# Kernel tuning notes

Hardware: AMD Instinct MI355X
Metric: run time of the kernel (lower is better)

Reference implementation:

```python
import jax, jax.numpy as jnp
import numpy as np

N_NODES = 50000
N_EDGES = 600000
D_IN = 128
D_HID = 128
D_OUT = 47
BN_EPS = 1e-5


def setup_inputs() -> dict:
    key = jax.random.key(0)
    ks = jax.random.split(key, 16)
    x = jax.random.normal(ks[0], (N_NODES, D_IN), dtype=jnp.float32)
    edge_index = jax.random.randint(ks[1], (2, N_EDGES), 0, N_NODES, dtype=jnp.int64)
    s = 0.05
    return {
        'x': x,
        'edge_index': edge_index,
        # SAGEConv layer 1: lin_l (neighbor agg, with bias), lin_r (root, no bias)
        'W1l': jax.random.normal(ks[2], (D_IN, D_HID), jnp.float32) * s,
        'b1': jnp.zeros((D_HID,), jnp.float32),
        'W1r': jax.random.normal(ks[3], (D_IN, D_HID), jnp.float32) * s,
        # layer 2
        'W2l': jax.random.normal(ks[4], (D_HID, D_HID), jnp.float32) * s,
        'b2': jnp.zeros((D_HID,), jnp.float32),
        'W2r': jax.random.normal(ks[5], (D_HID, D_HID), jnp.float32) * s,
        # layer 3
        'W3l': jax.random.normal(ks[6], (D_HID, D_OUT), jnp.float32) * s,
        'b3': jnp.zeros((D_OUT,), jnp.float32),
        'W3r': jax.random.normal(ks[7], (D_HID, D_OUT), jnp.float32) * s,
        # BatchNorm params (eval mode: running stats)
        'g1': jnp.ones((D_HID,), jnp.float32),
        'be1': jnp.zeros((D_HID,), jnp.float32),
        'm1': jax.random.normal(ks[8], (D_HID,), jnp.float32) * 0.1,
        'v1': jnp.ones((D_HID,), jnp.float32) + jax.random.uniform(ks[9], (D_HID,)) * 0.1,
        'g2': jnp.ones((D_HID,), jnp.float32),
        'be2': jnp.zeros((D_HID,), jnp.float32),
        'm2': jax.random.normal(ks[10], (D_HID,), jnp.float32) * 0.1,
        'v2': jnp.ones((D_HID,), jnp.float32) + jax.random.uniform(ks[11], (D_HID,)) * 0.1,
    }


def _sage_conv(x, src, dst, Wl, b, Wr):
    # mean aggregation of source features at destination nodes
    n = x.shape[0]
    msg = x[src]  # [E, d] gather
    agg = jax.ops.segment_sum(msg, dst, num_segments=n)
    cnt = jax.ops.segment_sum(jnp.ones((src.shape[0],), x.dtype), dst, num_segments=n)
    agg = agg / jnp.maximum(cnt, 1.0)[:, None]  # zero in-degree -> 0
    return agg @ Wl + b + x @ Wr


def _bn_eval(x, g, be, m, v):
    return (x - m) * (g * jax.lax.rsqrt(v + BN_EPS)) + be


def reference(x, edge_index, W1l, b1, W1r, W2l, b2, W2r, W3l, b3, W3r,
              g1, be1, m1, v1, g2, be2, m2, v2):
    src, dst = edge_index[0], edge_index[1]
    h = _sage_conv(x, src, dst, W1l, b1, W1r)
    h = jax.nn.relu(_bn_eval(h, g1, be1, m1, v1))  # dropout is identity in eval
    h = _sage_conv(h, src, dst, W2l, b2, W2r)
    h = jax.nn.relu(_bn_eval(h, g2, be2, m2, v2))
    return _sage_conv(h, src, dst, W3l, b3, W3r)
```

## Files before the change

kernel.cpp:

```cpp
#include <hip/hip_runtime.h>

#define NN 50000
#define NE 600000
#define D 128
#define DOUT3 47
#define ZW 64
#define BN_EPS 1e-5f
#define NPB 256
#define SB 196

typedef __attribute__((ext_vector_type(8))) short short8;
typedef __attribute__((ext_vector_type(4))) float f32x4;

__device__ inline unsigned short f2b(float f) {
  union { float f; unsigned u; } c; c.f = f;
  unsigned u = c.u;
  unsigned r = (u + 0x7FFFu + ((u >> 16) & 1u)) >> 16;
  return (unsigned short)r;
}
__device__ inline float b2f(unsigned short h) {
  union { unsigned u; float f; } c; c.u = ((unsigned)h) << 16;
  return c.f;
}

__global__ __launch_bounds__(256) void prep_kernel(
    const float4* __restrict__ x4, unsigned short* __restrict__ xb,
    int* __restrict__ deg,
    const float* __restrict__ W1l, const float* __restrict__ W1r, unsigned short* __restrict__ Bt1,
    const float* __restrict__ W2l, const float* __restrict__ W2r, unsigned short* __restrict__ Bt2,
    const float* __restrict__ W3l, const float* __restrict__ W3r, unsigned short* __restrict__ Bt3) {
  int b = blockIdx.x;
  int t = threadIdx.x;
  if (b < 1024) {
    long n4 = (long)NN * D / 4;
    for (long i = (long)b * 256 + t; i < n4; i += 1024L * 256) {
      float4 v = x4[i];
      uint2 p;
      p.x = (unsigned)f2b(v.x) | ((unsigned)f2b(v.y) << 16);
      p.y = (unsigned)f2b(v.z) | ((unsigned)f2b(v.w) << 16);
      *(uint2*)(xb + i * 4) = p;
    }
  } else if (b < 1220) {
    int i = (b - 1024) * 256 + t;
    if (i < NN) deg[i] = 0;
  } else if (b < 1476) {
    const float* Wl = (b < 1348) ? W1l : W2l;
    const float* Wr = (b < 1348) ? W1r : W2r;
    unsigned short* Bt = (b < 1348) ? Bt1 : Bt2;
    int idx = ((b < 1348) ? (b - 1220) : (b - 1348)) * 256 + t;
    int j = idx >> 8, k = idx & 255;
    float v = (k < 128) ? Wl[k * D + j] : Wr[(k - 128) * D + j];
    Bt[idx] = f2b(v);
  } else {
    int idx = (b - 1476) * 256 + t;
    if (idx < 112 * 128) {
      int j = idx >> 7, k = idx & 127;
      float v = 0.f;
      if (j < DOUT3) v = W3l[k * DOUT3 + j];
      else if (j >= 64 && j < 64 + DOUT3) v = W3r[k * DOUT3 + (j - 64)];
      Bt3[idx] = f2b(v);
    }
  }
}

__global__ void hist_kernel(const int* __restrict__ dst, int* __restrict__ deg, int E) {
  int e = blockIdx.x * blockDim.x + threadIdx.x;
  if (e < E) {
    int d = dst[e];
    d = max(0, min(NN - 1, d));
    atomicAdd(&deg[d], 1);
  }
}

__global__ __launch_bounds__(NPB) void scan_local(const int* __restrict__ deg,
                                                  int* __restrict__ row_start,
                                                  int* __restrict__ partials) {
  __shared__ int s[NPB];
  int t = threadIdx.x;
  int i = blockIdx.x * NPB + t;
  int v = (i < NN) ? deg[i] : 0;
  s[t] = v;
  __syncthreads();
  for (int off = 1; off < NPB; off <<= 1) {
    int u = (t >= off) ? s[t - off] : 0;
    __syncthreads();
    s[t] += u;
    __syncthreads();
  }
  if (i < NN) row_start[i] = s[t] - v;
  if (t == NPB - 1) partials[blockIdx.x] = s[NPB - 1];
}

__global__ __launch_bounds__(NPB) void scan_add(int* __restrict__ row_start,
                                                const int* __restrict__ partials,
                                                int* __restrict__ cursor) {
  __shared__ int s[NPB];
  int t = threadIdx.x;
  int v = (t < SB) ? partials[t] : 0;
  s[t] = v;
  __syncthreads();
  for (int off = 1; off < NPB; off <<= 1) {
    int u = (t >= off) ? s[t - off] : 0;
    __syncthreads();
    s[t] += u;
    __syncthreads();
  }
  int base = s[blockIdx.x] - partials[blockIdx.x];
  int i = blockIdx.x * NPB + t;
  if (i < NN) {
    int r = row_start[i] + base;
    row_start[i] = r;
    cursor[i] = r;
  }
  if (i == 0) row_start[NN] = NE;
}

__global__ void build_kernel(const int* __restrict__ src, const int* __restrict__ dst,
                             int* __restrict__ cursor, int* __restrict__ srcs, int E) {
  int e = blockIdx.x * blockDim.x + threadIdx.x;
  if (e < E) {
    int d = dst[e];
    d = max(0, min(NN - 1, d));
    int s = src[e];
    s = max(0, min(NN - 1, s));
    int pos = atomicAdd(&cursor[d], 1);
    srcs[pos] = s;
  }
}

__global__ __launch_bounds__(256) void gather_mean_b4(const unsigned short* __restrict__ feat,
                                                      const int* __restrict__ row_start,
                                                      const int* __restrict__ srcs,
                                                      unsigned short* __restrict__ agg) {
  int node = (blockIdx.x * blockDim.x + threadIdx.x) >> 6;
  int lane = threadIdx.x & 63;
  if (node >= NN) return;
  int g = lane >> 4, s = lane & 15;
  int start = row_start[node], end = row_start[node + 1];
  float a[8];
#pragma unroll
  for (int i = 0; i < 8; i++) a[i] = 0.f;
  const unsigned short* fp = feat + s * 8;
  for (int base = start; base < end; base += 64) {
    int cnt = min(end - base, 64);
    int idxv = (base + lane < end) ? srcs[base + lane] : 0;
    int M = (cnt + 3) >> 2;
    for (int m = 0; m < M; m += 2) {
      int e0 = m * 4 + g;
      int e1 = e0 + 4;
      int s0 = __shfl(idxv, e0);
      int s1 = __shfl(idxv, e1);
      float w0 = (e0 < cnt) ? 1.f : 0.f;
      float w1 = (e1 < cnt) ? 1.f : 0.f;
      short8 v0 = *(const short8*)(fp + (long)s0 * D);
      short8 v1 = *(const short8*)(fp + (long)s1 * D);
#pragma unroll
      for (int i = 0; i < 8; i++)
        a[i] += w0 * b2f((unsigned short)v0[i]) + w1 * b2f((unsigned short)v1[i]);
    }
  }
#pragma unroll
  for (int i = 0; i < 8; i++) {
    a[i] += __shfl_xor(a[i], 16);
    a[i] += __shfl_xor(a[i], 32);
  }
  if (g == 0) {
    float iv = 1.0f / fmaxf((float)(end - start), 1.0f);
    uint4 p;
    p.x = (unsigned)f2b(a[0] * iv) | ((unsigned)f2b(a[1] * iv) << 16);
    p.y = (unsigned)f2b(a[2] * iv) | ((unsigned)f2b(a[3] * iv) << 16);
    p.z = (unsigned)f2b(a[4] * iv) | ((unsigned)f2b(a[5] * iv) << 16);
    p.w = (unsigned)f2b(a[6] * iv) | ((unsigned)f2b(a[7] * iv) << 16);
    *(uint4*)(agg + (long)node * D + s * 8) = p;
  }
}

__global__ __launch_bounds__(256) void gather_add47(const unsigned short* __restrict__ Z,
                                                    const int* __restrict__ row_start,
                                                    const int* __restrict__ srcs,
                                                    float* __restrict__ outP) {
  int node = (blockIdx.x * blockDim.x + threadIdx.x) >> 6;
  int lane = threadIdx.x & 63;
  if (node >= NN) return;
  int g = lane >> 4, s = lane & 15;
  int start = row_start[node], end = row_start[node + 1];
  float a[4];
#pragma unroll
  for (int i = 0; i < 4; i++) a[i] = 0.f;
  const unsigned short* zp = Z + s * 4;
  for (int base = start; base < end; base += 64) {
    int cnt = min(end - base, 64);
    int idxv = (base + lane < end) ? srcs[base + lane] : 0;
    int M = (cnt + 3) >> 2;
    for (int m = 0; m < M; m += 2) {
      int e0 = m * 4 + g;
      int e1 = e0 + 4;
      int s0 = __shfl(idxv, e0);
      int s1 = __shfl(idxv, e1);
      float w0 = (e0 < cnt) ? 1.f : 0.f;
      float w1 = (e1 < cnt) ? 1.f : 0.f;
      uint2 u0 = *(const uint2*)(zp + (long)s0 * ZW);
      uint2 u1 = *(const uint2*)(zp + (long)s1 * ZW);
      a[0] += w0 * b2f((unsigned short)u0.x) + w1 * b2f((unsigned short)u1.x);
      a[1] += w0 * b2f((unsigned short)(u0.x >> 16)) + w1 * b2f((unsigned short)(u1.x >> 16));
      a[2] += w0 * b2f((unsigned short)u0.y) + w1 * b2f((unsigned short)u1.y);
      a[3] += w0 * b2f((unsigned short)(u0.y >> 16)) + w1 * b2f((unsigned short)(u1.y >> 16));
    }
  }
#pragma unroll
  for (int i = 0; i < 4; i++) {
    a[i] += __shfl_xor(a[i], 16);
    a[i] += __shfl_xor(a[i], 32);
  }
  if (g == 0) {
    float iv = 1.0f / fmaxf((float)(end - start), 1.0f);
#pragma unroll
    for (int i = 0; i < 4; i++) {
      int c = s * 4 + i;
      if (c < DOUT3) {
        long o = (long)node * DOUT3 + c;
        outP[o] = outP[o] + a[i] * iv;
      }
    }
  }
}

__global__ __launch_bounds__(256) void fused_mfma(
    const unsigned short* __restrict__ aggb, const unsigned short* __restrict__ xb,
    const unsigned short* __restrict__ Bt, const float* __restrict__ bias,
    const float* __restrict__ g, const float* __restrict__ be,
    const float* __restrict__ m, const float* __restrict__ v,
    unsigned short* __restrict__ outb, int tiles) {
  const int NF = 8;
  int wid = threadIdx.x >> 6, lane = threadIdx.x & 63;
  int tile = blockIdx.x * 4 + wid;
  if (tile >= tiles) return;
  int row0 = tile * 16;
  int r15 = lane & 15, hi = lane >> 4;

  f32x4 acc[NF];
#pragma unroll
  for (int f = 0; f < NF; f++) acc[f] = (f32x4)(0.f);

  const unsigned short* Arow_a = aggb + (long)(row0 + r15) * D + hi * 8;
  const unsigned short* Arow_x = xb + (long)(row0 + r15) * D + hi * 8;
  const unsigned short* Bp = Bt + (long)r15 * 256 + hi * 8;

#pragma unroll
  for (int kf = 0; kf < 8; kf++) {
    const int kk = kf * 32;
    short8 a = *(const short8*)((kf < 4 ? Arow_a : Arow_x) + (kk & 127));
#pragma unroll
    for (int f = 0; f < NF; f++) {
      short8 b = *(const short8*)(Bp + (long)f * 16 * 256 + kk);
      acc[f] = __builtin_amdgcn_mfma_f32_16x16x32_bf16(a, b, acc[f], 0, 0, 0);
    }
  }

#pragma unroll
  for (int f = 0; f < NF; f++) {
    int col = f * 16 + r15;
    float bj = bias[col];
    float sc = g[col] * rsqrtf(v[col] + BN_EPS);
    float sh = be[col] - m[col] * sc;
#pragma unroll
    for (int r = 0; r < 4; r++) {
      int row = row0 + hi * 4 + r;
      float val = fmaxf((acc[f][r] + bj) * sc + sh, 0.f);
      outb[(long)row * D + col] = f2b(val);
    }
  }
}

__global__ __launch_bounds__(256) void trans_mfma(
    const unsigned short* __restrict__ xb, const unsigned short* __restrict__ Bt3,
    const float* __restrict__ bias, unsigned short* __restrict__ Z,
    float* __restrict__ outP, int tiles) {
  const int NF = 7;
  int wid = threadIdx.x >> 6, lane = threadIdx.x & 63;
  int tile = blockIdx.x * 4 + wid;
  if (tile >= tiles) return;
  int row0 = tile * 16;
  int r15 = lane & 15, hi = lane >> 4;

  f32x4 acc[NF];
#pragma unroll
  for (int f = 0; f < NF; f++) acc[f] = (f32x4)(0.f);

  const unsigned short* Ar = xb + (long)(row0 + r15) * D + hi * 8;
  const unsigned short* Bp = Bt3 + (long)r15 * 128 + hi * 8;

#pragma unroll
  for (int kf = 0; kf < 4; kf++) {
    const int kk = kf * 32;
    short8 a = *(const short8*)(Ar + kk);
#pragma unroll
    for (int f = 0; f < NF; f++) {
      short8 b = *(const short8*)(Bp + (long)f * 16 * 128 + kk);
      acc[f] = __builtin_amdgcn_mfma_f32_16x16x32_bf16(a, b, acc[f], 0, 0, 0);
    }
  }

#pragma unroll
  for (int f = 0; f < NF; f++) {
    int col = f * 16 + r15;
#pragma unroll
    for (int r = 0; r < 4; r++) {
      int row = row0 + hi * 4 + r;
      float val = acc[f][r];
      if (col < ZW) {
        Z[(long)row * ZW + col] = f2b(val);
      } else {
        int pc = col - 64;
        if (pc < DOUT3) outP[(long)row * DOUT3 + pc] = val + bias[pc];
      }
    }
  }
}

extern "C" void kernel_launch(void* const* d_in, const int* in_sizes, int n_in,
                              void* d_out, int out_size, void* d_ws, size_t ws_size,
                              hipStream_t stream) {
  const float* x = (const float*)d_in[0];
  const int* ei = (const int*)d_in[1];
  const int* src = ei;
  const int* dst = ei + NE;
  const float* W1l = (const float*)d_in[2];
  const float* b1  = (const float*)d_in[3];
  const float* W1r = (const float*)d_in[4];
  const float* W2l = (const float*)d_in[5];
  const float* b2  = (const float*)d_in[6];
  const float* W2r = (const float*)d_in[7];
  const float* W3l = (const float*)d_in[8];
  const float* b3  = (const float*)d_in[9];
  const float* W3r = (const float*)d_in[10];
  const float* g1  = (const float*)d_in[11];
  const float* be1 = (const float*)d_in[12];
  const float* m1  = (const float*)d_in[13];
  const float* v1  = (const float*)d_in[14];
  const float* g2  = (const float*)d_in[15];
  const float* be2 = (const float*)d_in[16];
  const float* m2  = (const float*)d_in[17];
  const float* v2  = (const float*)d_in[18];

  float* out = (float*)d_out;

  int* deg       = (int*)d_ws;
  int* row_start = deg + NN;
  int* cursor    = row_start + NN + 4;
  int* partials  = cursor + NN;
  int* srcs      = partials + 256;
  unsigned short* xb   = (unsigned short*)(srcs + NE);
  unsigned short* aggb = xb + (long)NN * D;
  unsigned short* h1b  = aggb + (long)NN * D;
  unsigned short* Zb   = h1b + (long)NN * D;
  unsigned short* Bt1  = Zb + (long)NN * ZW;
  unsigned short* Bt2  = Bt1 + 128 * 256;
  unsigned short* Bt3  = Bt2 + 128 * 256;

  prep_kernel<<<1532, 256, 0, stream>>>(
      (const float4*)x, xb, deg, W1l, W1r, Bt1, W2l, W2r, Bt2, W3l, W3r, Bt3);

  hist_kernel<<<(NE + 255) / 256, 256, 0, stream>>>(dst, deg, NE);
  scan_local<<<SB, NPB, 0, stream>>>(deg, row_start, partials);
  scan_add<<<SB, NPB, 0, stream>>>(row_start, partials, cursor);
  build_kernel<<<(NE + 255) / 256, 256, 0, stream>>>(src, dst, cursor, srcs, NE);

  int gather_blocks = (NN * 64 + 255) / 256;
  int tiles = NN / 16;
  int mfma_blocks = (tiles + 3) / 4;

  gather_mean_b4<<<gather_blocks, 256, 0, stream>>>(xb, row_start, srcs, aggb);
  fused_mfma<<<mfma_blocks, 256, 0, stream>>>(
      aggb, xb, Bt1, b1, g1, be1, m1, v1, h1b, tiles);

  gather_mean_b4<<<gather_blocks, 256, 0, stream>>>(h1b, row_start, srcs, aggb);
  fused_mfma<<<mfma_blocks, 256, 0, stream>>>(
      aggb, h1b, Bt2, b2, g2, be2, m2, v2, h1b, tiles);

  trans_mfma<<<mfma_blocks, 256, 0, stream>>>(h1b, Bt3, b3, Zb, out, tiles);
  gather_add47<<<gather_blocks, 256, 0, stream>>>(Zb, row_start, srcs, out);
}
```

Baseline: 253.7 us.

## Fuse neighbor mean-gather into MFMA layer kernel via shared memory

Merges the gather-mean aggregation into the SAGE layer MFMA kernel. Each wave gathers its 16-node tile into LDS and feeds it straight to the MFMA, so the bf16 aggregate no longer makes a round trip through global memory and two launches are dropped. The gather now uses 16 lanes per node instead of a full wave, and gather_add47 is reworked the same way. The histogram is folded into the prep kernel, with a separate zeroing kernel added beforehand. A second output buffer is used because layer 2 now reads neighbor rows that it would otherwise overwrite. The trade-off is less memory-level parallelism per node: each wave walks its 16 nodes in four serial rounds.

```diff
diff --git a/kernel.cpp b/kernel.cpp
--- a/kernel.cpp
+++ b/kernel.cpp
@@ -23,12 +23,17 @@
   return c.f;
 }
 
-__global__ __launch_bounds__(256) void prep_kernel(
+__global__ void zero_int(int* __restrict__ p, int n) {
+  int i = blockIdx.x * blockDim.x + threadIdx.x;
+  if (i < n) p[i] = 0;
+}
+
+__global__ __launch_bounds__(256) void prep_hist(
     const float4* __restrict__ x4, unsigned short* __restrict__ xb,
-    int* __restrict__ deg,
     const float* __restrict__ W1l, const float* __restrict__ W1r, unsigned short* __restrict__ Bt1,
     const float* __restrict__ W2l, const float* __restrict__ W2r, unsigned short* __restrict__ Bt2,
-    const float* __restrict__ W3l, const float* __restrict__ W3r, unsigned short* __restrict__ Bt3) {
+    const float* __restrict__ W3l, const float* __restrict__ W3r, unsigned short* __restrict__ Bt3,
+    const int* __restrict__ dst, int* __restrict__ deg) {
   int b = blockIdx.x;
   int t = threadIdx.x;
   if (b < 1024) {
@@ -40,19 +45,16 @@
       p.y = (unsigned)f2b(v.z) | ((unsigned)f2b(v.w) << 16);
       *(uint2*)(xb + i * 4) = p;
     }
-  } else if (b < 1220) {
-    int i = (b - 1024) * 256 + t;
-    if (i < NN) deg[i] = 0;
-  } else if (b < 1476) {
-    const float* Wl = (b < 1348) ? W1l : W2l;
-    const float* Wr = (b < 1348) ? W1r : W2r;
-    unsigned short* Bt = (b < 1348) ? Bt1 : Bt2;
-    int idx = ((b < 1348) ? (b - 1220) : (b - 1348)) * 256 + t;
+  } else if (b < 1280) {
+    const float* Wl = (b < 1152) ? W1l : W2l;
+    const float* Wr = (b < 1152) ? W1r : W2r;
+    unsigned short* Bt = (b < 1152) ? Bt1 : Bt2;
+    int idx = ((b < 1152) ? (b - 1024) : (b - 1152)) * 256 + t;
     int j = idx >> 8, k = idx & 255;
     float v = (k < 128) ? Wl[k * D + j] : Wr[(k - 128) * D + j];
     Bt[idx] = f2b(v);
-  } else {
-    int idx = (b - 1476) * 256 + t;
+  } else if (b < 1336) {
+    int idx = (b - 1280) * 256 + t;
     if (idx < 112 * 128) {
       int j = idx >> 7, k = idx & 127;
       float v = 0.f;
@@ -60,15 +62,13 @@
       else if (j >= 64 && j < 64 + DOUT3) v = W3r[k * DOUT3 + (j - 64)];
       Bt3[idx] = f2b(v);
     }
-  }
-}
-
-__global__ void hist_kernel(const int* __restrict__ dst, int* __restrict__ deg, int E) {
-  int e = blockIdx.x * blockDim.x + threadIdx.x;
-  if (e < E) {
-    int d = dst[e];
-    d = max(0, min(NN - 1, d));
-    atomicAdd(&deg[d], 1);
+  } else {
+    int e = (b - 1336) * 256 + t;
+    if (e < NE) {
+      int d = dst[e];
+      d = max(0, min(NN - 1, d));
+      atomicAdd(&deg[d], 1);
+    }
   }
 }
 
@@ -128,137 +128,77 @@
   }
 }
 
-__global__ __launch_bounds__(256) void gather_mean_b4(const unsigned short* __restrict__ feat,
-                                                      const int* __restrict__ row_start,
-                                                      const int* __restrict__ srcs,
-                                                      unsigned short* __restrict__ agg) {
-  int node = (blockIdx.x * blockDim.x + threadIdx.x) >> 6;
-  int lane = threadIdx.x & 63;
-  if (node >= NN) return;
-  int g = lane >> 4, s = lane & 15;
-  int start = row_start[node], end = row_start[node + 1];
-  float a[8];
-#pragma unroll
-  for (int i = 0; i < 8; i++) a[i] = 0.f;
+__global__ __launch_bounds__(256) void fused_gather_mfma(
+    const unsigned short* __restrict__ feat,
+    const int* __restrict__ row_start, const int* __restrict__ srcs,
+    const unsigned short* __restrict__ Bt, const float* __restrict__ bias,
+    const float* __restrict__ g, const float* __restrict__ be,
+    const float* __restrict__ m, const float* __restrict__ v,
+    unsigned short* __restrict__ outb, int tiles) {
+  __shared__ __align__(16) unsigned short s_a[4][16][136];
+  int wid = threadIdx.x >> 6, lane = threadIdx.x & 63;
+  int tile = blockIdx.x * 4 + wid;
+  tile = min(tile, tiles - 1);
+  int row0 = tile * 16;
+  int grp = lane >> 4, s = lane & 15;
   const unsigned short* fp = feat + s * 8;
-  for (int base = start; base < end; base += 64) {
-    int cnt = min(end - base, 64);
-    int idxv = (base + lane < end) ? srcs[base + lane] : 0;
-    int M = (cnt + 3) >> 2;
-    for (int m = 0; m < M; m += 2) {
-      int e0 = m * 4 + g;
-      int e1 = e0 + 4;
-      int s0 = __shfl(idxv, e0);
-      int s1 = __shfl(idxv, e1);
-      float w0 = (e0 < cnt) ? 1.f : 0.f;
-      float w1 = (e1 < cnt) ? 1.f : 0.f;
-      short8 v0 = *(const short8*)(fp + (long)s0 * D);
-      short8 v1 = *(const short8*)(fp + (long)s1 * D);
-#pragma unroll
-      for (int i = 0; i < 8; i++)
-        a[i] += w0 * b2f((unsigned short)v0[i]) + w1 * b2f((unsigned short)v1[i]);
-    }
-  }
-#pragma unroll
-  for (int i = 0; i < 8; i++) {
-    a[i] += __shfl_xor(a[i], 16);
-    a[i] += __shfl_xor(a[i], 32);
-  }
-  if (g == 0) {
+
+  for (int n = 0; n < 4; n++) {
+    int node = row0 + n * 4 + grp;
+    int start = row_start[node], end = row_start[node + 1];
+    float a[8];
+#pragma unroll
+    for (int i = 0; i < 8; i++) a[i] = 0.f;
+    for (int base = start; base < end; base += 16) {
+      int cnt = min(end - base, 16);
+      int idxv = (base + s < end) ? srcs[base + s] : 0;
+      int M = (cnt + 1) >> 1;
+      for (int mm = 0; mm < M; mm++) {
+        int e0 = mm * 2, e1 = e0 + 1;
+        int s0 = __shfl(idxv, e0, 16);
+        int s1 = __shfl(idxv, e1, 16);
+        float w1 = (e1 < cnt) ? 1.f : 0.f;
+        short8 v0 = *(const short8*)(fp + (long)s0 * D);
+        short8 v1 = *(const short8*)(fp + (long)s1 * D);
+#pragma unroll
+        for (int i = 0; i < 8; i++)
+          a[i] += b2f((unsigned short)v0[i]) + w1 * b2f((unsigned short)v1[i]);
+      }
+    }
     float iv = 1.0f / fmaxf((float)(end - start), 1.0f);
     uint4 p;
     p.x = (unsigned)f2b(a[0] * iv) | ((unsigned)f2b(a[1] * iv) << 16);
     p.y = (unsigned)f2b(a[2] * iv) | ((unsigned)f2b(a[3] * iv) << 16);
     p.z = (unsigned)f2b(a[4] * iv) | ((unsigned)f2b(a[5] * iv) << 16);
     p.w = (unsigned)f2b(a[6] * iv) | ((unsigned)f2b(a[7] * iv) << 16);
-    *(uint4*)(agg + (long)node * D + s * 8) = p;
-  }
-}
-
-__global__ __launch_bounds__(256) void gather_add47(const unsigned short* __restrict__ Z,
-                                                    const int* __restrict__ row_start,
-                                                    const int* __restrict__ srcs,
-                                                    float* __restrict__ outP) {
-  int node = (blockIdx.x * blockDim.x + threadIdx.x) >> 6;
-  int lane = threadIdx.x & 63;
-  if (node >= NN) return;
-  int g = lane >> 4, s = lane & 15;
-  int start = row_start[node], end = row_start[node + 1];
-  float a[4];
-#pragma unroll
-  for (int i = 0; i < 4; i++) a[i] = 0.f;
-  const unsigned short* zp = Z + s * 4;
-  for (int base = start; base < end; base += 64) {
-    int cnt = min(end - base, 64);
-    int idxv = (base + lane < end) ? srcs[base + lane] : 0;
-    int M = (cnt + 3) >> 2;
-    for (int m = 0; m < M; m += 2) {
-      int e0 = m * 4 + g;
-      int e1 = e0 + 4;
-      int s0 = __shfl(idxv, e0);
-      int s1 = __shfl(idxv, e1);
-      float w0 = (e0 < cnt) ? 1.f : 0.f;
-      float w1 = (e1 < cnt) ? 1.f : 0.f;
-      uint2 u0 = *(const uint2*)(zp + (long)s0 * ZW);
-      uint2 u1 = *(const uint2*)(zp + (long)s1 * ZW);
-      a[0] += w0 * b2f((unsigned short)u0.x) + w1 * b2f((unsigned short)u1.x);
-      a[1] += w0 * b2f((unsigned short)(u0.x >> 16)) + w1 * b2f((unsigned short)(u1.x >> 16));
-      a[2] += w0 * b2f((unsigned short)u0.y) + w1 * b2f((unsigned short)u1.y);
-      a[3] += w0 * b2f((unsigned short)(u0.y >> 16)) + w1 * b2f((unsigned short)(u1.y >> 16));
-    }
-  }
-#pragma unroll
-  for (int i = 0; i < 4; i++) {
-    a[i] += __shfl_xor(a[i], 16);
-    a[i] += __shfl_xor(a[i], 32);
-  }
-  if (g == 0) {
-    float iv = 1.0f / fmaxf((float)(end - start), 1.0f);
-#pragma unroll
-    for (int i = 0; i < 4; i++) {
-      int c = s * 4 + i;
-      if (c < DOUT3) {
-        long o = (long)node * DOUT3 + c;
-        outP[o] = outP[o] + a[i] * iv;
-      }
-    }
-  }
-}
-
-__global__ __launch_bounds__(256) void fused_mfma(
-    const unsigned short* __restrict__ aggb, const unsigned short* __restrict__ xb,
-    const unsigned short* __restrict__ Bt, const float* __restrict__ bias,
-    const float* __restrict__ g, const float* __restrict__ be,
-    const float* __restrict__ m, const float* __restrict__ v,
-    unsigned short* __restrict__ outb, int tiles) {
-  const int NF = 8;
-  int wid = threadIdx.x >> 6, lane = threadIdx.x & 63;
-  int tile = blockIdx.x * 4 + wid;
-  if (tile >= tiles) return;
-  int row0 = tile * 16;
-  int r15 = lane & 15, hi = lane >> 4;
-
-  f32x4 acc[NF];
-#pragma unroll
-  for (int f = 0; f < NF; f++) acc[f] = (f32x4)(0.f);
-
-  const unsigned short* Arow_a = aggb + (long)(row0 + r15) * D + hi * 8;
-  const unsigned short* Arow_x = xb + (long)(row0 + r15) * D + hi * 8;
+    *(uint4*)&s_a[wid][n * 4 + grp][s * 8] = p;
+  }
+
+  __syncthreads();
+
+  int r15 = s, hi = grp;
+  f32x4 acc[8];
+#pragma unroll
+  for (int f = 0; f < 8; f++) acc[f] = (f32x4)(0.f);
+
+  const unsigned short* As = &s_a[wid][r15][hi * 8];
+  const unsigned short* Ax = feat + (long)(row0 + r15) * D + hi * 8;
   const unsigned short* Bp = Bt + (long)r15 * 256 + hi * 8;
 
 #pragma unroll
   for (int kf = 0; kf < 8; kf++) {
     const int kk = kf * 32;
-    short8 a = *(const short8*)((kf < 4 ? Arow_a : Arow_x) + (kk & 127));
-#pragma unroll
-    for (int f = 0; f < NF; f++) {
+    short8 a = (kf < 4) ? *(const short8*)(As + kk)
+                        : *(const short8*)(Ax + (kk - 128));
+#pragma unroll
+    for (int f = 0; f < 8; f++) {
       short8 b = *(const short8*)(Bp + (long)f * 16 * 256 + kk);
       acc[f] = __builtin_amdgcn_mfma_f32_16x16x32_bf16(a, b, acc[f], 0, 0, 0);
     }
   }
 
 #pragma unroll
-  for (int f = 0; f < NF; f++) {
+  for (int f = 0; f < 8; f++) {
     int col = f * 16 + r15;
     float bj = bias[col];
     float sc = g[col] * rsqrtf(v[col] + BN_EPS);
@@ -314,6 +254,47 @@
         int pc = col - 64;
         if (pc < DOUT3) outP[(long)row * DOUT3 + pc] = val + bias[pc];
       }
+    }
+  }
+}
+
+__global__ __launch_bounds__(256) void gather_add47(const unsigned short* __restrict__ Z,
+                                                    const int* __restrict__ row_start,
+                                                    const int* __restrict__ srcs,
+                                                    float* __restrict__ outP) {
+  int t = blockIdx.x * blockDim.x + threadIdx.x;
+  int node = t >> 4;
+  int s = t & 15;
+  if (node >= NN) return;
+  int start = row_start[node], end = row_start[node + 1];
+  float a[4];
+#pragma unroll
+  for (int i = 0; i < 4; i++) a[i] = 0.f;
+  const unsigned short* zp = Z + s * 4;
+  for (int base = start; base < end; base += 16) {
+    int cnt = min(end - base, 16);
+    int idxv = (base + s < end) ? srcs[base + s] : 0;
+    int M = (cnt + 1) >> 1;
+    for (int mm = 0; mm < M; mm++) {
+      int e0 = mm * 2, e1 = e0 + 1;
+      int s0 = __shfl(idxv, e0, 16);
+      int s1 = __shfl(idxv, e1, 16);
+      float w1 = (e1 < cnt) ? 1.f : 0.f;
+      uint2 u0 = *(const uint2*)(zp + (long)s0 * ZW);
+      uint2 u1 = *(const uint2*)(zp + (long)s1 * ZW);
+      a[0] += b2f((unsigned short)u0.x) + w1 * b2f((unsigned short)u1.x);
+      a[1] += b2f((unsigned short)(u0.x >> 16)) + w1 * b2f((unsigned short)(u1.x >> 16));
+      a[2] += b2f((unsigned short)u0.y) + w1 * b2f((unsigned short)u1.y);
+      a[3] += b2f((unsigned short)(u0.y >> 16)) + w1 * b2f((unsigned short)(u1.y >> 16));
+    }
+  }
+  float iv = 1.0f / fmaxf((float)(end - start), 1.0f);
+#pragma unroll
+  for (int i = 0; i < 4; i++) {
+    int c = s * 4 + i;
+    if (c < DOUT3) {
+      long o = (long)node * DOUT3 + c;
+      outP[o] = outP[o] + a[i] * iv;
     }
   }
 }
@@ -351,33 +332,30 @@
   int* partials  = cursor + NN;
   int* srcs      = partials + 256;
   unsigned short* xb   = (unsigned short*)(srcs + NE);
-  unsigned short* aggb = xb + (long)NN * D;
-  unsigned short* h1b  = aggb + (long)NN * D;
+  unsigned short* h2b  = xb + (long)NN * D;
+  unsigned short* h1b  = h2b + (long)NN * D;
   unsigned short* Zb   = h1b + (long)NN * D;
   unsigned short* Bt1  = Zb + (long)NN * ZW;
   unsigned short* Bt2  = Bt1 + 128 * 256;
   unsigned short* Bt3  = Bt2 + 128 * 256;
 
-  prep_kernel<<<1532, 256, 0, stream>>>(
-      (const float4*)x, xb, deg, W1l, W1r, Bt1, W2l, W2r, Bt2, W3l, W3r, Bt3);
-
-  hist_kernel<<<(NE + 255) / 256, 256, 0, stream>>>(dst, deg, NE);
+  zero_int<<<SB, 256, 0, stream>>>(deg, NN);
+  prep_hist<<<3680, 256, 0, stream>>>(
+      (const float4*)x, xb, W1l, W1r, Bt1, W2l, W2r, Bt2, W3l, W3r, Bt3, dst, deg);
+
   scan_local<<<SB, NPB, 0, stream>>>(deg, row_start, partials);
   scan_add<<<SB, NPB, 0, stream>>>(row_start, partials, cursor);
   build_kernel<<<(NE + 255) / 256, 256, 0, stream>>>(src, dst, cursor, srcs, NE);
 
-  int gather_blocks = (NN * 64 + 255) / 256;
   int tiles = NN / 16;
-  int mfma_blocks = (tiles + 3) / 4;
-
-  gather_mean_b4<<<gather_blocks, 256, 0, stream>>>(xb, row_start, srcs, aggb);
-  fused_mfma<<<mfma_blocks, 256, 0, stream>>>(
-      aggb, xb, Bt1, b1, g1, be1, m1, v1, h1b, tiles);
-
-  gather_mean_b4<<<gather_blocks, 256, 0, stream>>>(h1b, row_start, srcs, aggb);
-  fused_mfma<<<mfma_blocks, 256, 0, stream>>>(
-      aggb, h1b, Bt2, b2, g2, be2, m2, v2, h1b, tiles);
-
-  trans_mfma<<<mfma_blocks, 256, 0, stream>>>(h1b, Bt3, b3, Zb, out, tiles);
-  gather_add47<<<gather_blocks, 256, 0, stream>>>(Zb, row_start, srcs, out);
-}
+  int lblocks = (tiles + 3) / 4;
+
+  fused_gather_mfma<<<lblocks, 256, 0, stream>>>(
+      xb, row_start, srcs, Bt1, b1, g1, be1, m1, v1, h1b, tiles);
+
+  fused_gather_mfma<<<lblocks, 256, 0, stream>>>(
+      h1b, row_start, srcs, Bt2, b2, g2, be2, m2, v2, h2b, tiles);
+
+  trans_mfma<<<lblocks, 256, 0, stream>>>(h2b, Bt3, b3, Zb, out, tiles);
+  gather_add47<<<(NN * 16 + 255) / 256, 256, 0, stream>>>(Zb, row_start, srcs, out);
+}
```

Result: faster. 237.1 us (-6.5%).
